# Kernel optimization log

Hardware: AMD Instinct MI355X
Metric: run time of the kernel (lower is better)

The kernel has to match this reference:

```python
import jax, jax.numpy as jnp
import numpy as np

DIM_IN, DIM_H, DIM_OUT = 1024, 512, 256
E, T, B = 8, 4, 16384


def setup_inputs() -> dict:
    key = jax.random.key(0)
    ks = jax.random.split(key, 8)
    s1 = 1.0 / np.sqrt(DIM_IN)
    s2 = 1.0 / np.sqrt(DIM_H)
    x = jax.random.normal(ks[0], (B, DIM_IN), dtype=jnp.float32)
    # stacked expert params: layer1 [E, H, IN], layer2 [E, OUT, H]
    W1 = jax.random.uniform(ks[1], (E, DIM_H, DIM_IN), jnp.float32, -s1, s1)
    b1 = jax.random.uniform(ks[2], (E, DIM_H), jnp.float32, -s1, s1)
    W2 = jax.random.uniform(ks[3], (E, DIM_OUT, DIM_H), jnp.float32, -s2, s2)
    b2 = jax.random.uniform(ks[4], (E, DIM_OUT), jnp.float32, -s2, s2)
    # gate params: [T, E, IN]
    Wg = jax.random.uniform(ks[5], (T, E, DIM_IN), jnp.float32, -s1, s1)
    bg = jax.random.uniform(ks[6], (T, E), jnp.float32, -s1, s1)
    return {"x": x, "W1": W1, "b1": b1, "W2": W2, "b2": b2, "Wg": Wg, "bg": bg}


def reference(x, W1, b1, W2, b2, Wg, bg):
    # Experts: Linear+ReLU, Linear+ReLU (dropout=0 / eval mode)
    h = jax.nn.relu(jnp.einsum('bi,ehi->beh', x, W1) + b1)          # [B,E,H]
    feats = jax.nn.relu(jnp.einsum('beh,edh->bed', h, W2) + b2)     # [B,E,D]
    # Gates: softmax over experts, one gate per task
    logits = jnp.einsum('bi,tei->bte', x, Wg) + bg                  # [B,T,E]
    w = jax.nn.softmax(logits, axis=-1)                             # [B,T,E]
    # Weighted combine: einsum('bde,be->bd') per task
    out = jnp.einsum('bed,bte->tbd', feats, w)                      # [T,B,D]
    return out
```

## Files before the change

### kernel.cpp

```cpp
#include <hip/hip_runtime.h>


typedef __attribute__((ext_vector_type(8))) __bf16 bf16x8;
typedef __attribute__((ext_vector_type(4))) float f32x4;
typedef __attribute__((ext_vector_type(8))) unsigned short u16x8;

__device__ __forceinline__ float bf2f(unsigned short u) {
  union { unsigned int i; float f; } x;
  x.i = ((unsigned int)u) << 16;
  return x.f;
}

__device__ __forceinline__ unsigned short f2bf(float f) {
  union { float f; unsigned int i; } x;
  x.f = f;
  unsigned int r = x.i + 0x7FFFu + ((x.i >> 16) & 1u);
  return (unsigned short)(r >> 16);
}

__device__ __forceinline__ void gload_lds16(const unsigned short* g, unsigned short* l) {
  __builtin_amdgcn_global_load_lds(
      (const __attribute__((address_space(1))) void*)g,
      (__attribute__((address_space(3))) void*)l, 16, 0, 0);
}

__global__ void cvt_k(const float* __restrict__ in, unsigned short* __restrict__ out, int n4) {
  int i = blockIdx.x * blockDim.x + threadIdx.x;
  if (i >= n4) return;
  float4 v = ((const float4*)in)[i];
  ushort4 o;
  o.x = f2bf(v.x); o.y = f2bf(v.y); o.z = f2bf(v.z); o.w = f2bf(v.w);
  ((ushort4*)out)[i] = o;
}

__global__ __launch_bounds__(256) void gates_k(
    const unsigned short* __restrict__ xb,
    const unsigned short* __restrict__ Wgb,
    const float* __restrict__ bg,
    float* __restrict__ gw)
{
  const int lane = threadIdx.x & 63;
  const int wid = threadIdx.x >> 6;
  const int wgid = blockIdx.x * 4 + wid;
  const int brow = wgid * 16;
  const int l15 = lane & 15, lhi = lane >> 4;

  f32x4 acc0 = {0.f, 0.f, 0.f, 0.f};
  f32x4 acc1 = {0.f, 0.f, 0.f, 0.f};
  for (int k0 = 0; k0 < 1024; k0 += 32) {
    bf16x8 a  = *(const bf16x8*)&xb[(size_t)(brow + l15) * 1024 + k0 + lhi * 8];
    bf16x8 b0 = *(const bf16x8*)&Wgb[(size_t)l15 * 1024 + k0 + lhi * 8];
    bf16x8 b1 = *(const bf16x8*)&Wgb[(size_t)(16 + l15) * 1024 + k0 + lhi * 8];
    acc0 = __builtin_amdgcn_mfma_f32_16x16x32_bf16(a, b0, acc0, 0, 0, 0);
    acc1 = __builtin_amdgcn_mfma_f32_16x16x32_bf16(a, b1, acc1, 0, 0, 0);
  }
  const float bg0 = bg[l15];
  const float bg1 = bg[16 + l15];
#pragma unroll
  for (int r = 0; r < 4; ++r) {
    float v0 = acc0[r] + bg0;
    float v1 = acc1[r] + bg1;
    float m0 = v0, m1 = v1;
#pragma unroll
    for (int d = 1; d <= 4; d <<= 1) {
      m0 = fmaxf(m0, __shfl_xor(m0, d));
      m1 = fmaxf(m1, __shfl_xor(m1, d));
    }
    float e0 = __expf(v0 - m0), e1 = __expf(v1 - m1);
    float s0 = e0, s1 = e1;
#pragma unroll
    for (int d = 1; d <= 4; d <<= 1) {
      s0 += __shfl_xor(s0, d);
      s1 += __shfl_xor(s1, d);
    }
    int b = brow + lhi * 4 + r;
    gw[(size_t)b * 32 + l15]      = e0 / s0;
    gw[(size_t)b * 32 + 16 + l15] = e1 / s1;
  }
}

template <bool RELU>
__global__ __launch_bounds__(256) void gemm_bt(
    const unsigned short* __restrict__ A, int lda, int aZ,
    const unsigned short* __restrict__ B,
    const float* __restrict__ bias,
    unsigned short* __restrict__ C, int ldc, int cZ,
    int N, int K)
{
  __shared__ unsigned short As[128 * 64];
  __shared__ unsigned short Bs[128 * 64];
  const int tid = threadIdx.x;
  const int wid = tid >> 6;
  const int lane = tid & 63;
  const int wr = wid >> 1, wc = wid & 1;
  const int l15 = lane & 15, lhi = lane >> 4;
  const int brow = blockIdx.x * 128;
  const int bcol = blockIdx.y * 128;
  const int e = blockIdx.z;

  const unsigned short* Ab = A + (size_t)e * aZ;
  const unsigned short* Bb = B + (size_t)e * N * K;
  const float* biasb = bias + (size_t)e * N;
  unsigned short* Cb = C + (size_t)e * cZ;

  const f32x4 zero = {0.f, 0.f, 0.f, 0.f};
  f32x4 acc[4][4];
#pragma unroll
  for (int m = 0; m < 4; ++m)
#pragma unroll
    for (int n = 0; n < 4; ++n) acc[m][n] = zero;

  const int srow = lane >> 3;
  const int scol = (lane & 7) * 8;
  const int rbase = wid * 32;

  for (int k0 = 0; k0 < K; k0 += 64) {
#pragma unroll
    for (int i = 0; i < 4; ++i) {
      int r = rbase + i * 8;
      gload_lds16(Ab + (size_t)(brow + r + srow) * lda + (k0 + scol), &As[r * 64]);
    }
#pragma unroll
    for (int i = 0; i < 4; ++i) {
      int r = rbase + i * 8;
      gload_lds16(Bb + (size_t)(bcol + r + srow) * K + (k0 + scol), &Bs[r * 64]);
    }
    __syncthreads();
#pragma unroll
    for (int kk = 0; kk < 2; ++kk) {
      bf16x8 af[4], bfr[4];
#pragma unroll
      for (int m = 0; m < 4; ++m)
        af[m] = *(const bf16x8*)&As[(wr * 64 + m * 16 + l15) * 64 + kk * 32 + lhi * 8];
#pragma unroll
      for (int n = 0; n < 4; ++n)
        bfr[n] = *(const bf16x8*)&Bs[(wc * 64 + n * 16 + l15) * 64 + kk * 32 + lhi * 8];
#pragma unroll
      for (int m = 0; m < 4; ++m)
#pragma unroll
        for (int n = 0; n < 4; ++n)
          acc[m][n] = __builtin_amdgcn_mfma_f32_16x16x32_bf16(af[m], bfr[n], acc[m][n], 0, 0, 0);
    }
    __syncthreads();
  }

#pragma unroll
  for (int n = 0; n < 4; ++n) {
    int col = bcol + wc * 64 + n * 16 + l15;
    float bv = biasb[col];
#pragma unroll
    for (int m = 0; m < 4; ++m) {
      int row0 = brow + wr * 64 + m * 16 + lhi * 4;
#pragma unroll
      for (int r = 0; r < 4; ++r) {
        float v = acc[m][n][r] + bv;
        if (RELU) v = v > 0.f ? v : 0.f;
        Cb[(size_t)(row0 + r) * ldc + col] = f2bf(v);
      }
    }
  }
}

__global__ __launch_bounds__(256) void combine_k(
    const unsigned short* __restrict__ feats,
    const float* __restrict__ gw,
    float* __restrict__ out)
{
  int tid = blockIdx.x * 256 + threadIdx.x;
  int b = tid >> 5;
  int d0 = (tid & 31) * 8;

  const f32x4* wv4 = (const f32x4*)(gw + (size_t)b * 32);
  f32x4 wv[8];
#pragma unroll
  for (int i = 0; i < 8; ++i) wv[i] = wv4[i];

  float o[4][8];
#pragma unroll
  for (int t = 0; t < 4; ++t)
#pragma unroll
    for (int j = 0; j < 8; ++j) o[t][j] = 0.f;

#pragma unroll
  for (int e = 0; e < 8; ++e) {
    u16x8 fv = *(const u16x8*)&feats[((size_t)b * 8 + e) * 256 + d0];
    float f[8];
#pragma unroll
    for (int j = 0; j < 8; ++j) f[j] = bf2f(fv[j]);
#pragma unroll
    for (int t = 0; t < 4; ++t) {
      float wt = wv[(t * 8 + e) >> 2][(t * 8 + e) & 3];
#pragma unroll
      for (int j = 0; j < 8; ++j) o[t][j] += wt * f[j];
    }
  }
#pragma unroll
  for (int t = 0; t < 4; ++t) {
    f32x4* dst = (f32x4*)(out + ((size_t)t * 16384 + b) * 256 + d0);
    f32x4 s0 = {o[t][0], o[t][1], o[t][2], o[t][3]};
    f32x4 s1 = {o[t][4], o[t][5], o[t][6], o[t][7]};
    dst[0] = s0;
    dst[1] = s1;
  }
}

extern "C" void kernel_launch(void* const* d_in, const int* in_sizes, int n_in,
                              void* d_out, int out_size, void* d_ws, size_t ws_size,
                              hipStream_t stream) {
  (void)in_sizes; (void)n_in; (void)out_size; (void)ws_size;
  const float* x  = (const float*)d_in[0];
  const float* W1 = (const float*)d_in[1];
  const float* b1 = (const float*)d_in[2];
  const float* W2 = (const float*)d_in[3];
  const float* b2 = (const float*)d_in[4];
  const float* Wg = (const float*)d_in[5];
  const float* bg = (const float*)d_in[6];
  float* out = (float*)d_out;

  char* ws = (char*)d_ws;
  unsigned short* xb    = (unsigned short*)ws; ws += (size_t)16384 * 1024 * 2;
  unsigned short* W1b   = (unsigned short*)ws; ws += (size_t)4096 * 1024 * 2;
  unsigned short* W2b   = (unsigned short*)ws; ws += (size_t)2048 * 512 * 2;
  unsigned short* Wgb   = (unsigned short*)ws; ws += (size_t)32 * 1024 * 2;
  float*          gw    = (float*)ws;         ws += (size_t)16384 * 32 * 4;
  unsigned short* H     = (unsigned short*)ws; ws += (size_t)16384 * 4096 * 2;
  unsigned short* feats = (unsigned short*)ws; ws += (size_t)16384 * 2048 * 2;

  cvt_k<<<16384, 256, 0, stream>>>(x, xb, 16384 * 1024 / 4);
  cvt_k<<<4096, 256, 0, stream>>>(W1, W1b, 4096 * 1024 / 4);
  cvt_k<<<1024, 256, 0, stream>>>(W2, W2b, 2048 * 512 / 4);
  cvt_k<<<32, 256, 0, stream>>>(Wg, Wgb, 32 * 1024 / 4);

  gates_k<<<256, 256, 0, stream>>>(xb, Wgb, bg, gw);

  gemm_bt<true><<<dim3(128, 32, 1), 256, 0, stream>>>(
      xb, 1024, 0, W1b, b1, H, 4096, 0, 4096, 1024);

  gemm_bt<true><<<dim3(128, 2, 8), 256, 0, stream>>>(
      H, 4096, 512, W2b, b2, feats, 2048, 256, 256, 512);

  combine_k<<<2048, 256, 0, stream>>>(feats, gw, out);
}
```

Baseline: 339.5 us.

## Rewrite expert GEMMs as 256x256 double-buffered swizzled-LDS kernel with prefetch

Replaces the 128x128 single-buffered GEMM with a 256x256 tile, 512-thread kernel that double-buffers K-tiles in 128KB of dynamic LDS. Next-tile loads are issued mid-iteration between MFMA phases, and wave priority is raised around the MFMA blocks. It also XOR-swizzles the LDS layout to avoid bank conflicts, remaps workgroups for L2 locality, and vectorizes bias loads and output stores. The aim is to hide global-load latency and raise MFMA utilization, at the cost of heavy LDS use per workgroup (occupancy limited) and more complex barrier and waitcnt logic.

```diff
diff --git a/kernel.cpp b/kernel.cpp
--- a/kernel.cpp
+++ b/kernel.cpp
@@ -22,6 +22,24 @@
   __builtin_amdgcn_global_load_lds(
       (const __attribute__((address_space(1))) void*)g,
       (__attribute__((address_space(3))) void*)l, 16, 0, 0);
+}
+
+__device__ __forceinline__ void stage_half(const unsigned short* gbase, int gld,
+                                           unsigned short* region, int wid, int lane) {
+#pragma unroll
+  for (int c = 0; c < 2; ++c) {
+    int d = ((wid * 64 + lane) << 4) + (c << 13);
+    int row = d >> 7;
+    int gr = ((d >> 4) & 7) ^ (row & 7);
+    gload_lds16(gbase + (size_t)row * gld + (gr << 3),
+                region + ((wid << 9) + (c << 12)));
+  }
+}
+
+__device__ __forceinline__ bf16x8 frag_ld(const unsigned short* region, int row, int kk, int lhi) {
+  int byte = (row << 7) + (kk << 6) + (lhi << 4);
+  byte ^= (row & 7) << 4;
+  return *(const bf16x8*)((const char*)region + byte);
 }
 
 __global__ void cvt_k(const float* __restrict__ in, unsigned short* __restrict__ out, int n4) {
@@ -80,22 +98,27 @@
 }
 
 template <bool RELU>
-__global__ __launch_bounds__(256) void gemm_bt(
+__global__ __launch_bounds__(512, 2) void gemm256(
     const unsigned short* __restrict__ A, int lda, int aZ,
     const unsigned short* __restrict__ B,
     const float* __restrict__ bias,
     unsigned short* __restrict__ C, int ldc, int cZ,
-    int N, int K)
+    int tilesN, int N, int K)
 {
-  __shared__ unsigned short As[128 * 64];
-  __shared__ unsigned short Bs[128 * 64];
+  extern __shared__ char smem_raw[];
+  unsigned short* lds = (unsigned short*)smem_raw;
+
   const int tid = threadIdx.x;
-  const int wid = tid >> 6;
-  const int lane = tid & 63;
-  const int wr = wid >> 1, wc = wid & 1;
+  const int lane = tid & 63, wid = tid >> 6;
+  const int wr = wid >> 2, wc = wid & 3;
   const int l15 = lane & 15, lhi = lane >> 4;
-  const int brow = blockIdx.x * 128;
-  const int bcol = blockIdx.y * 128;
+
+  const int nwg = gridDim.x;
+  const int cpx = nwg >> 3;
+  const int wg = blockIdx.x;
+  const int swz = (wg & 7) * cpx + (wg >> 3);
+  const int rt = swz / tilesN, ct = swz - rt * tilesN;
+  const int brow = rt * 256, bcol = ct * 256;
   const int e = blockIdx.z;
 
   const unsigned short* Ab = A + (size_t)e * aZ;
@@ -103,60 +126,154 @@
   const float* biasb = bias + (size_t)e * N;
   unsigned short* Cb = C + (size_t)e * cZ;
 
+  const int NT = K >> 6;
+
+  f32x4 bias4[4];
+#pragma unroll
+  for (int nf = 0; nf < 4; ++nf)
+    bias4[nf] = *(const f32x4*)&biasb[bcol + wc * 64 + nf * 16 + lhi * 4];
+
   const f32x4 zero = {0.f, 0.f, 0.f, 0.f};
-  f32x4 acc[4][4];
-#pragma unroll
-  for (int m = 0; m < 4; ++m)
+  f32x4 acc[8][4];
+#pragma unroll
+  for (int m = 0; m < 8; ++m)
 #pragma unroll
     for (int n = 0; n < 4; ++n) acc[m][n] = zero;
 
-  const int srow = lane >> 3;
-  const int scol = (lane & 7) * 8;
-  const int rbase = wid * 32;
-
-  for (int k0 = 0; k0 < K; k0 += 64) {
-#pragma unroll
-    for (int i = 0; i < 4; ++i) {
-      int r = rbase + i * 8;
-      gload_lds16(Ab + (size_t)(brow + r + srow) * lda + (k0 + scol), &As[r * 64]);
-    }
-#pragma unroll
-    for (int i = 0; i < 4; ++i) {
-      int r = rbase + i * 8;
-      gload_lds16(Bb + (size_t)(bcol + r + srow) * K + (k0 + scol), &Bs[r * 64]);
-    }
-    __syncthreads();
-#pragma unroll
-    for (int kk = 0; kk < 2; ++kk) {
-      bf16x8 af[4], bfr[4];
-#pragma unroll
-      for (int m = 0; m < 4; ++m)
-        af[m] = *(const bf16x8*)&As[(wr * 64 + m * 16 + l15) * 64 + kk * 32 + lhi * 8];
-#pragma unroll
-      for (int n = 0; n < 4; ++n)
-        bfr[n] = *(const bf16x8*)&Bs[(wc * 64 + n * 16 + l15) * 64 + kk * 32 + lhi * 8];
-#pragma unroll
-      for (int m = 0; m < 4; ++m)
-#pragma unroll
-        for (int n = 0; n < 4; ++n)
-          acc[m][n] = __builtin_amdgcn_mfma_f32_16x16x32_bf16(af[m], bfr[n], acc[m][n], 0, 0, 0);
-    }
-    __syncthreads();
-  }
-
-#pragma unroll
-  for (int n = 0; n < 4; ++n) {
-    int col = bcol + wc * 64 + n * 16 + l15;
-    float bv = biasb[col];
-#pragma unroll
-    for (int m = 0; m < 4; ++m) {
-      int row0 = brow + wr * 64 + m * 16 + lhi * 4;
-#pragma unroll
-      for (int r = 0; r < 4; ++r) {
-        float v = acc[m][n][r] + bv;
-        if (RELU) v = v > 0.f ? v : 0.f;
-        Cb[(size_t)(row0 + r) * ldc + col] = f2bf(v);
+#pragma unroll
+  for (int tt = 0; tt < 2; ++tt) {
+#pragma unroll
+    for (int h = 0; h < 2; ++h)
+      stage_half(Ab + (size_t)(brow + h * 128) * lda + tt * 64, lda,
+                 lds + (tt * 4 + h) * 8192, wid, lane);
+#pragma unroll
+    for (int h = 0; h < 2; ++h)
+      stage_half(Bb + (size_t)(bcol + h * 128) * K + tt * 64, K,
+                 lds + (tt * 4 + 2 + h) * 8192, wid, lane);
+  }
+  asm volatile("s_waitcnt vmcnt(8)" ::: "memory");
+  __builtin_amdgcn_s_barrier();
+
+  const int bro = (wc & 1) * 64;
+
+#pragma unroll 1
+  for (int t = 0; t < NT; ++t) {
+    const int b = t & 1;
+    const unsigned short* Ar = lds + (b * 4 + wr) * 8192;
+    const unsigned short* Br = lds + (b * 4 + 2 + (wc >> 1)) * 8192;
+
+    bf16x8 af0[4][2], af1[4][2], bf0[2][2], bf1[2][2];
+
+#pragma unroll
+    for (int m = 0; m < 4; ++m)
+#pragma unroll
+      for (int kk = 0; kk < 2; ++kk)
+        af0[m][kk] = frag_ld(Ar, m * 16 + l15, kk, lhi);
+#pragma unroll
+    for (int n = 0; n < 2; ++n)
+#pragma unroll
+      for (int kk = 0; kk < 2; ++kk)
+        bf0[n][kk] = frag_ld(Br, bro + n * 16 + l15, kk, lhi);
+    __builtin_amdgcn_s_barrier();
+    __builtin_amdgcn_s_setprio(1);
+#pragma unroll
+    for (int m = 0; m < 4; ++m)
+#pragma unroll
+      for (int n = 0; n < 2; ++n)
+#pragma unroll
+        for (int kk = 0; kk < 2; ++kk)
+          acc[m][n] = __builtin_amdgcn_mfma_f32_16x16x32_bf16(bf0[n][kk], af0[m][kk], acc[m][n], 0, 0, 0);
+    __builtin_amdgcn_s_setprio(0);
+    __builtin_amdgcn_s_barrier();
+
+#pragma unroll
+    for (int n = 0; n < 2; ++n)
+#pragma unroll
+      for (int kk = 0; kk < 2; ++kk)
+        bf1[n][kk] = frag_ld(Br, bro + (2 + n) * 16 + l15, kk, lhi);
+#pragma unroll
+    for (int m = 0; m < 4; ++m)
+#pragma unroll
+      for (int kk = 0; kk < 2; ++kk)
+        af1[m][kk] = frag_ld(Ar, (4 + m) * 16 + l15, kk, lhi);
+    __builtin_amdgcn_s_barrier();
+    __builtin_amdgcn_s_setprio(1);
+#pragma unroll
+    for (int m = 0; m < 4; ++m)
+#pragma unroll
+      for (int n = 0; n < 2; ++n)
+#pragma unroll
+        for (int kk = 0; kk < 2; ++kk)
+          acc[m][2 + n] = __builtin_amdgcn_mfma_f32_16x16x32_bf16(bf1[n][kk], af0[m][kk], acc[m][2 + n], 0, 0, 0);
+    __builtin_amdgcn_s_setprio(0);
+    __builtin_amdgcn_s_barrier();
+
+    if (t + 2 < NT) {
+      const int kt = t + 2;
+#pragma unroll
+      for (int h = 0; h < 2; ++h)
+        stage_half(Ab + (size_t)(brow + h * 128) * lda + kt * 64, lda,
+                   lds + (b * 4 + h) * 8192, wid, lane);
+    }
+    __builtin_amdgcn_s_barrier();
+    __builtin_amdgcn_s_setprio(1);
+#pragma unroll
+    for (int m = 0; m < 4; ++m)
+#pragma unroll
+      for (int n = 0; n < 2; ++n)
+#pragma unroll
+        for (int kk = 0; kk < 2; ++kk)
+          acc[4 + m][n] = __builtin_amdgcn_mfma_f32_16x16x32_bf16(bf0[n][kk], af1[m][kk], acc[4 + m][n], 0, 0, 0);
+    __builtin_amdgcn_s_setprio(0);
+    __builtin_amdgcn_s_barrier();
+
+    if (t + 2 < NT) {
+      const int kt = t + 2;
+#pragma unroll
+      for (int h = 0; h < 2; ++h)
+        stage_half(Bb + (size_t)(bcol + h * 128) * K + kt * 64, K,
+                   lds + (b * 4 + 2 + h) * 8192, wid, lane);
+    }
+    __builtin_amdgcn_s_barrier();
+    __builtin_amdgcn_s_setprio(1);
+#pragma unroll
+    for (int m = 0; m < 4; ++m)
+#pragma unroll
+      for (int n = 0; n < 2; ++n)
+#pragma unroll
+        for (int kk = 0; kk < 2; ++kk)
+          acc[4 + m][2 + n] = __builtin_amdgcn_mfma_f32_16x16x32_bf16(bf1[n][kk], af1[m][kk], acc[4 + m][2 + n], 0, 0, 0);
+    __builtin_amdgcn_s_setprio(0);
+
+    if (t + 2 < NT) {
+      asm volatile("s_waitcnt vmcnt(8)" ::: "memory");
+      __builtin_amdgcn_s_barrier();
+    } else if (t + 1 < NT) {
+      asm volatile("s_waitcnt vmcnt(0)" ::: "memory");
+      __builtin_amdgcn_s_barrier();
+    }
+  }
+
+#pragma unroll
+  for (int mf = 0; mf < 8; ++mf) {
+    const size_t rowoff = (size_t)(brow + wr * 128 + mf * 16 + l15) * ldc;
+#pragma unroll
+    for (int nf = 0; nf < 4; ++nf) {
+      const int col = bcol + wc * 64 + nf * 16 + lhi * 4;
+      f32x4 v = acc[mf][nf];
+      ushort4 o;
+      float v0 = v[0] + bias4[nf][0];
+      float v1 = v[1] + bias4[nf][1];
+      float v2 = v[2] + bias4[nf][2];
+      float v3 = v[3] + bias4[nf][3];
+      if (RELU) {
+        v0 = v0 > 0.f ? v0 : 0.f;
+        v1 = v1 > 0.f ? v1 : 0.f;
+        v2 = v2 > 0.f ? v2 : 0.f;
+        v3 = v3 > 0.f ? v3 : 0.f;
       }
+      o.x = f2bf(v0); o.y = f2bf(v1); o.z = f2bf(v2); o.w = f2bf(v3);
+      *(ushort4*)&Cb[rowoff + col] = o;
     }
   }
 }
@@ -233,11 +350,11 @@
 
   gates_k<<<256, 256, 0, stream>>>(xb, Wgb, bg, gw);
 
-  gemm_bt<true><<<dim3(128, 32, 1), 256, 0, stream>>>(
-      xb, 1024, 0, W1b, b1, H, 4096, 0, 4096, 1024);
-
-  gemm_bt<true><<<dim3(128, 2, 8), 256, 0, stream>>>(
-      H, 4096, 512, W2b, b2, feats, 2048, 256, 256, 512);
+  gemm256<true><<<dim3(1024, 1, 1), 512, 131072, stream>>>(
+      xb, 1024, 0, W1b, b1, H, 4096, 0, 16, 4096, 1024);
+
+  gemm256<true><<<dim3(64, 1, 8), 512, 131072, stream>>>(
+      H, 4096, 512, W2b, b2, feats, 2048, 256, 1, 256, 512);
 
   combine_k<<<2048, 256, 0, stream>>>(feats, gw, out);
 }
```

Result: slower. 418.8 us (+23.4%).
